# Kernel optimization log

Measured on AMD Instinct MI355X. Metric: run time of the kernel, lower is better.

The kernel has to match this reference:

```python
import jax, jax.numpy as jnp
import numpy as np

RANK, A1, A2, B1, B2 = 64, 64, 64, 64, 64
N_TOKENS = 8192


def _xavier_uniform(key, shape, fan_in, fan_out, dtype=jnp.float32):
    bound = float(np.sqrt(6.0 / (fan_in + fan_out)))
    return jax.random.uniform(key, shape, dtype, -bound, bound)


def setup_inputs() -> dict:
    key = jax.random.key(0)
    kx, ka, kb, kbias = jax.random.split(key, 4)
    x = jax.random.normal(kx, (N_TOKENS, A1 * B1), dtype=jnp.float32)
    # torch xavier on a 3D tensor (rank, d1, d2): fan_in = d1*d2, fan_out = rank*d2
    a = _xavier_uniform(ka, (RANK, A1, A2), A1 * A2, RANK * A2)
    b = _xavier_uniform(kb, (RANK, B1, B2), B1 * B2, RANK * B2)
    bias = jax.random.normal(kbias, (A2 * B2,), dtype=jnp.float32)
    return {"x": x, "a": a, "b": b, "bias": bias}


def reference(x, a, b, bias):
    r, a1, a2 = a.shape
    _, b1, b2 = b.shape
    # w = sum_r kron(a_r, b_r):  w[i*b1+k, j*b2+l] = sum_r a[r,i,j] * b[r,k,l]
    w = jnp.einsum('rij,rkl->ikjl', a, b).reshape(a1 * b1, a2 * b2)
    out = x @ w  # (N, a2*b2)
    return out + bias[None, :]
```

## Files before the change

kernel.cpp:

```cpp
#include <hip/hip_runtime.h>
#include <hip/hip_bf16.h>


#define M_DIM 8192
#define N_DIM 4096
#define K_DIM 4096
#define KT_COUNT 128

typedef __attribute__((ext_vector_type(8))) short short8;
typedef __attribute__((ext_vector_type(4))) float floatx4;

typedef __attribute__((address_space(1))) void gvoid_t;
typedef __attribute__((address_space(3))) void lvoid_t;

static __device__ __forceinline__ void gl_lds16(const void* g, const void* l) {
  __builtin_amdgcn_global_load_lds((gvoid_t*)(unsigned long long)g,
                                   (lvoid_t*)(unsigned int)(unsigned long long)l,
                                   16, 0, 0);
}

static __device__ __forceinline__ unsigned short f2bf(float f) {
  unsigned int u = __builtin_bit_cast(unsigned int, f);
  u = (u + 0x7fffu + ((u >> 16) & 1u)) >> 16;
  return (unsigned short)u;
}

#define BAR() asm volatile("s_barrier" ::: "memory")
#define WAIT_VM(N) asm volatile("s_waitcnt vmcnt(" #N ")" ::: "memory")
#define WAIT_LGKM0() asm volatile("s_waitcnt lgkmcnt(0)" ::: "memory")

__global__ __launch_bounds__(256) void build_w_kernel(
    const float* __restrict__ a, const float* __restrict__ b,
    unsigned short* __restrict__ Wp) {
  __shared__ float lds_a[1024];
  __shared__ float lds_b[2][4096];
  const int bid = blockIdx.x;
  const int t = threadIdx.x;
  const int rg = bid & 255;
  const int i = rg >> 2;
  const int j0 = (rg & 3) * 16;
  const int k0 = (bid >> 8) * 8;

  {
    const int r = t >> 2, jq = t & 3;
    float4 v = ((const float4*)(a + (size_t)r * 4096 + i * 64 + j0))[jq];
    ((float4*)lds_a)[r * 4 + jq] = v;
  }

  const float* bsrc = b + k0 * 64;

#pragma unroll
  for (int p = 0; p < 4; ++p) {
    const int idx = p * 256 + t;
    gl_lds16(bsrc + (size_t)(idx >> 7) * 4096 + (idx & 127) * 4,
             &((float4*)lds_b[0])[idx]);
  }
  WAIT_VM(0);
  __syncthreads();

  const int l = t & 63;
  const int jj = t >> 6;
  float acc[4][8];
#pragma unroll
  for (int jp = 0; jp < 4; ++jp)
#pragma unroll
    for (int kb = 0; kb < 8; ++kb) acc[jp][kb] = 0.f;

  for (int g = 0; g < 8; ++g) {
    const int cur = g & 1;
    if (g < 7) {
      const float* nb = bsrc + (size_t)(g + 1) * 8 * 4096;
#pragma unroll
      for (int p = 0; p < 4; ++p) {
        const int idx = p * 256 + t;
        gl_lds16(nb + (size_t)(idx >> 7) * 4096 + (idx & 127) * 4,
                 &((float4*)lds_b[cur ^ 1])[idx]);
      }
    }
#pragma unroll
    for (int rr = 0; rr < 8; ++rr) {
      float4 aj = ((const float4*)lds_a)[(g * 8 + rr) * 4 + jj];
      float bv[8];
#pragma unroll
      for (int kb = 0; kb < 8; ++kb) bv[kb] = lds_b[cur][rr * 512 + kb * 64 + l];
      const float av[4] = {aj.x, aj.y, aj.z, aj.w};
#pragma unroll
      for (int jp = 0; jp < 4; ++jp)
#pragma unroll
        for (int kb = 0; kb < 8; ++kb)
          acc[jp][kb] = fmaf(av[jp], bv[kb], acc[jp][kb]);
    }
    WAIT_VM(0);
    __syncthreads();
  }

  const int kt = (i * 64 + k0) >> 5;
  const int cw = (k0 & 31) >> 3;
#pragma unroll
  for (int jp = 0; jp < 4; ++jp) {
    const int j = j0 + jj * 4 + jp;
    const int n = j * 64 + l;
    const int blob = (n >> 7) * KT_COUNT + kt;
    const int pos = cw * 128 + (n & 127);
    short8 o;
#pragma unroll
    for (int kb = 0; kb < 8; ++kb) o[kb] = (short)f2bf(acc[jp][kb]);
    *(short8*)(Wp + (size_t)blob * 4096 + pos * 8) = o;
  }
}

__global__ __launch_bounds__(512) void pack_x_kernel(
    const float* __restrict__ x, unsigned short* __restrict__ Xp) {
  __shared__ short8 smem[2048];
  const int pid = blockIdx.x;
  const int M0 = pid >> 5;
  const int h = (pid >> 4) & 1;
  const int kg = pid & 15;
  const int t = threadIdx.x;

  {
    const int rsub = t >> 5;
    const int col8 = t & 31;
#pragma unroll
    for (int p = 0; p < 4; ++p) {
      const int rr = p * 16 + rsub;
      const float* src =
          x + (size_t)(M0 * 128 + h * 64 + rr) * K_DIM + kg * 256 + col8 * 8;
      float4 v0 = ((const float4*)src)[0];
      float4 v1 = ((const float4*)src)[1];
      short8 o;
      o[0] = (short)f2bf(v0.x); o[1] = (short)f2bf(v0.y);
      o[2] = (short)f2bf(v0.z); o[3] = (short)f2bf(v0.w);
      o[4] = (short)f2bf(v1.x); o[5] = (short)f2bf(v1.y);
      o[6] = (short)f2bf(v1.z); o[7] = (short)f2bf(v1.w);
      smem[rr * 32 + (col8 ^ (rr & 31))] = o;
    }
  }
  __syncthreads();

  const int ml = t & 63;
  const int c = (t >> 6) & 3;
  const int qh = t >> 8;
#pragma unroll
  for (int q = 0; q < 4; ++q) {
    const int qq = q * 2 + qh;
    const int cc = qq * 4 + c;
    short8 v = smem[ml * 32 + (cc ^ (ml & 31))];
    unsigned short* dst = Xp + (size_t)(M0 * KT_COUNT + kg * 8 + qq) * 4096 +
                          (size_t)(c * 128 + h * 64 + ml) * 8;
    *(short8*)dst = v;
  }
}

__global__ __launch_bounds__(512, 2) void gemm_kernel(
    const unsigned short* __restrict__ Xp, const unsigned short* __restrict__ Wp,
    const float* __restrict__ bias, float* __restrict__ out) {
  __shared__ short8 As[4][2][512];
  __shared__ short8 Bs[4][2][512];

  const int bid = blockIdx.x;
  const int xcd = bid & 7;
  const int pos = bid >> 3;
  const int N0 = xcd * 2 + (pos & 1);
  const int M0 = pos >> 1;

  const int t = threadIdx.x;
  const int wave = t >> 6, lane = t & 63;
  const int l16 = lane & 15, quad = lane >> 4;
  const int wm = wave & 1;
  const int wn = wave >> 1;

  floatx4 acc[8][4];
#pragma unroll
  for (int mt = 0; mt < 8; ++mt)
#pragma unroll
    for (int nt = 0; nt < 4; ++nt) acc[mt][nt] = (floatx4){0.f, 0.f, 0.f, 0.f};

  const unsigned short* gA0 = Xp + (size_t)(M0 * 2 + 0) * KT_COUNT * 4096 + (size_t)t * 8;
  const unsigned short* gA1 = Xp + (size_t)(M0 * 2 + 1) * KT_COUNT * 4096 + (size_t)t * 8;
  const unsigned short* gB0 = Wp + (size_t)(N0 * 2 + 0) * KT_COUNT * 4096 + (size_t)t * 8;
  const unsigned short* gB1 = Wp + (size_t)(N0 * 2 + 1) * KT_COUNT * 4096 + (size_t)t * 8;

  gl_lds16(gA0, &As[0][0][t]);
  gl_lds16(gA1, &As[0][1][t]);
  gl_lds16(gB0, &Bs[0][0][t]);
  gl_lds16(gB1, &Bs[0][1][t]);
  gl_lds16(gA0 + 4096, &As[1][0][t]);
  gl_lds16(gA1 + 4096, &As[1][1][t]);
  gl_lds16(gB0 + 4096, &Bs[1][0][t]);
  gl_lds16(gB1 + 4096, &Bs[1][1][t]);
  WAIT_VM(4);
  BAR();

  const int ra = quad * 128 + l16;
  const int rb = quad * 128 + (wn & 1) * 64 + l16;
  const int bh = wn >> 1;

#pragma unroll 2
  for (int kt = 0; kt < KT_COUNT; ++kt) {
    const int tb = kt & 3;
    const int db = (kt + 2) & 3;
    const size_t soff =
        (size_t)((kt + 2 < KT_COUNT) ? kt + 2 : KT_COUNT - 1) * 4096;

    short8 bf[4], af[4];

#pragma unroll
    for (int nt = 0; nt < 4; ++nt) bf[nt] = Bs[tb][bh][rb + nt * 16];
#pragma unroll
    for (int m = 0; m < 4; ++m) af[m] = As[tb][wm][ra + m * 16];
    gl_lds16(gA0 + soff, &As[db][0][t]);
    gl_lds16(gA1 + soff, &As[db][1][t]);
    BAR();
    WAIT_LGKM0();
    __builtin_amdgcn_sched_barrier(0);
    __builtin_amdgcn_s_setprio(1);
#pragma unroll
    for (int m = 0; m < 4; ++m)
#pragma unroll
      for (int nt = 0; nt < 4; ++nt)
        acc[m][nt] = __builtin_amdgcn_mfma_f32_16x16x32_bf16(
            af[m], bf[nt], acc[m][nt], 0, 0, 0);
    __builtin_amdgcn_s_setprio(0);
    __builtin_amdgcn_sched_barrier(0);
    BAR();

#pragma unroll
    for (int m = 0; m < 4; ++m) af[m] = As[tb][wm][ra + (4 + m) * 16];
    gl_lds16(gB0 + soff, &Bs[db][0][t]);
    gl_lds16(gB1 + soff, &Bs[db][1][t]);
    WAIT_VM(4);
    BAR();
    WAIT_LGKM0();
    __builtin_amdgcn_sched_barrier(0);
    __builtin_amdgcn_s_setprio(1);
#pragma unroll
    for (int m = 0; m < 4; ++m)
#pragma unroll
      for (int nt = 0; nt < 4; ++nt)
        acc[4 + m][nt] = __builtin_amdgcn_mfma_f32_16x16x32_bf16(
            af[m], bf[nt], acc[4 + m][nt], 0, 0, 0);
    __builtin_amdgcn_s_setprio(0);
    __builtin_amdgcn_sched_barrier(0);
    BAR();
  }

  const int col_base = N0 * 256 + wn * 64;
  const int row_base = M0 * 256 + wm * 128;
#pragma unroll
  for (int nt = 0; nt < 4; ++nt) {
    const int col = col_base + nt * 16 + l16;
    const float bv = bias[col];
#pragma unroll
    for (int mt = 0; mt < 8; ++mt) {
      floatx4 v = acc[mt][nt];
#pragma unroll
      for (int r4 = 0; r4 < 4; ++r4) {
        const int row = row_base + mt * 16 + quad * 4 + r4;
        out[(size_t)row * N_DIM + col] = v[r4] + bv;
      }
    }
  }
}

extern "C" void kernel_launch(void* const* d_in, const int* in_sizes, int n_in,
                              void* d_out, int out_size, void* d_ws, size_t ws_size,
                              hipStream_t stream) {
  const float* x = (const float*)d_in[0];
  const float* a = (const float*)d_in[1];
  const float* b = (const float*)d_in[2];
  const float* bias = (const float*)d_in[3];
  float* out = (float*)d_out;

  unsigned short* Xp = (unsigned short*)d_ws;
  unsigned short* Wp = Xp + (size_t)M_DIM * K_DIM;

  build_w_kernel<<<2048, 256, 0, stream>>>(a, b, Wp);
  pack_x_kernel<<<2048, 512, 0, stream>>>(x, Xp);
  gemm_kernel<<<512, 512, 0, stream>>>(Xp, Wp, bias, out);
}
```

Measured before the change: 474.2 us.

## Restructure W build for register reuse and enlarge X pack tiles

Result: slower. 489.9 us (+3.3%).

```diff
diff --git a/kernel.cpp b/kernel.cpp
--- a/kernel.cpp
+++ b/kernel.cpp
@@ -29,92 +29,92 @@
 #define WAIT_VM(N) asm volatile("s_waitcnt vmcnt(" #N ")" ::: "memory")
 #define WAIT_LGKM0() asm volatile("s_waitcnt lgkmcnt(0)" ::: "memory")
 
-__global__ __launch_bounds__(256) void build_w_kernel(
+__global__ __launch_bounds__(512, 2) void build_w_kernel(
     const float* __restrict__ a, const float* __restrict__ b,
     unsigned short* __restrict__ Wp) {
-  __shared__ float lds_a[1024];
-  __shared__ float lds_b[2][4096];
+  __shared__ float lds_a[4096];
   const int bid = blockIdx.x;
+  const int i = bid >> 2;
+  const int kq = bid & 3;
   const int t = threadIdx.x;
-  const int rg = bid & 255;
-  const int i = rg >> 2;
-  const int j0 = (rg & 3) * 16;
-  const int k0 = (bid >> 8) * 8;
-
-  {
-    const int r = t >> 2, jq = t & 3;
-    float4 v = ((const float4*)(a + (size_t)r * 4096 + i * 64 + j0))[jq];
-    ((float4*)lds_a)[r * 4 + jq] = v;
-  }
-
-  const float* bsrc = b + k0 * 64;
-
-#pragma unroll
-  for (int p = 0; p < 4; ++p) {
-    const int idx = p * 256 + t;
-    gl_lds16(bsrc + (size_t)(idx >> 7) * 4096 + (idx & 127) * 4,
-             &((float4*)lds_b[0])[idx]);
+  const int kbh = t >> 8;
+  const int j4 = (t >> 4) & 15;
+  const int l4 = t & 15;
+
+#pragma unroll
+  for (int p = 0; p < 2; ++p) {
+    const int idx = p * 512 + t;
+    const int r = idx >> 4, jq = idx & 15;
+    gl_lds16(a + (size_t)r * 4096 + i * 64 + jq * 4, &((float4*)lds_a)[idx]);
   }
   WAIT_VM(0);
   __syncthreads();
 
-  const int l = t & 63;
-  const int jj = t >> 6;
-  float acc[4][8];
+  float acc[4][4][8];
 #pragma unroll
   for (int jp = 0; jp < 4; ++jp)
 #pragma unroll
-    for (int kb = 0; kb < 8; ++kb) acc[jp][kb] = 0.f;
-
-  for (int g = 0; g < 8; ++g) {
-    const int cur = g & 1;
-    if (g < 7) {
-      const float* nb = bsrc + (size_t)(g + 1) * 8 * 4096;
-#pragma unroll
-      for (int p = 0; p < 4; ++p) {
-        const int idx = p * 256 + t;
-        gl_lds16(nb + (size_t)(idx >> 7) * 4096 + (idx & 127) * 4,
-                 &((float4*)lds_b[cur ^ 1])[idx]);
-      }
+    for (int lp = 0; lp < 4; ++lp)
+#pragma unroll
+      for (int kbi = 0; kbi < 8; ++kbi) acc[jp][lp][kbi] = 0.f;
+
+  const float* bb = b + (kq * 16 + kbh * 8) * 64 + l4 * 4;
+
+  float4 bv0[8], bv1[8];
+#pragma unroll
+  for (int kbi = 0; kbi < 8; ++kbi)
+    bv0[kbi] = *(const float4*)(bb + kbi * 64);
+
+#define BW_FMA(AV, BV)                                                   \
+  do {                                                                   \
+    const float av_[4] = {(AV).x, (AV).y, (AV).z, (AV).w};               \
+    _Pragma("unroll") for (int jp = 0; jp < 4; ++jp) {                   \
+      _Pragma("unroll") for (int kbi = 0; kbi < 8; ++kbi) {              \
+        acc[jp][0][kbi] = fmaf(av_[jp], (BV)[kbi].x, acc[jp][0][kbi]);   \
+        acc[jp][1][kbi] = fmaf(av_[jp], (BV)[kbi].y, acc[jp][1][kbi]);   \
+        acc[jp][2][kbi] = fmaf(av_[jp], (BV)[kbi].z, acc[jp][2][kbi]);   \
+        acc[jp][3][kbi] = fmaf(av_[jp], (BV)[kbi].w, acc[jp][3][kbi]);   \
+      }                                                                  \
+    }                                                                    \
+  } while (0)
+
+  for (int r = 0; r < 64; r += 2) {
+    const float* b1 = bb + (size_t)(r + 1) * 4096;
+#pragma unroll
+    for (int kbi = 0; kbi < 8; ++kbi) bv1[kbi] = *(const float4*)(b1 + kbi * 64);
+    float4 av0 = *(const float4*)&lds_a[r * 64 + j4 * 4];
+    BW_FMA(av0, bv0);
+    const int r2 = (r + 2 < 64) ? r + 2 : 0;
+    const float* b2 = bb + (size_t)r2 * 4096;
+#pragma unroll
+    for (int kbi = 0; kbi < 8; ++kbi) bv0[kbi] = *(const float4*)(b2 + kbi * 64);
+    float4 av1 = *(const float4*)&lds_a[(r + 1) * 64 + j4 * 4];
+    BW_FMA(av1, bv1);
+  }
+#undef BW_FMA
+
+  const int kt = i * 2 + (kq >> 1);
+  const int c = (kq & 1) * 2 + kbh;
+#pragma unroll
+  for (int jp = 0; jp < 4; ++jp) {
+#pragma unroll
+    for (int lp = 0; lp < 4; ++lp) {
+      const int n = (j4 * 4 + jp) * 64 + l4 * 4 + lp;
+      const int blob = (n >> 7) * KT_COUNT + kt;
+      const int pos = c * 128 + (n & 127);
+      short8 o;
+#pragma unroll
+      for (int kbi = 0; kbi < 8; ++kbi) o[kbi] = (short)f2bf(acc[jp][lp][kbi]);
+      *(short8*)(Wp + (size_t)blob * 4096 + pos * 8) = o;
     }
-#pragma unroll
-    for (int rr = 0; rr < 8; ++rr) {
-      float4 aj = ((const float4*)lds_a)[(g * 8 + rr) * 4 + jj];
-      float bv[8];
-#pragma unroll
-      for (int kb = 0; kb < 8; ++kb) bv[kb] = lds_b[cur][rr * 512 + kb * 64 + l];
-      const float av[4] = {aj.x, aj.y, aj.z, aj.w};
-#pragma unroll
-      for (int jp = 0; jp < 4; ++jp)
-#pragma unroll
-        for (int kb = 0; kb < 8; ++kb)
-          acc[jp][kb] = fmaf(av[jp], bv[kb], acc[jp][kb]);
-    }
-    WAIT_VM(0);
-    __syncthreads();
-  }
-
-  const int kt = (i * 64 + k0) >> 5;
-  const int cw = (k0 & 31) >> 3;
-#pragma unroll
-  for (int jp = 0; jp < 4; ++jp) {
-    const int j = j0 + jj * 4 + jp;
-    const int n = j * 64 + l;
-    const int blob = (n >> 7) * KT_COUNT + kt;
-    const int pos = cw * 128 + (n & 127);
-    short8 o;
-#pragma unroll
-    for (int kb = 0; kb < 8; ++kb) o[kb] = (short)f2bf(acc[jp][kb]);
-    *(short8*)(Wp + (size_t)blob * 4096 + pos * 8) = o;
   }
 }
 
 __global__ __launch_bounds__(512) void pack_x_kernel(
     const float* __restrict__ x, unsigned short* __restrict__ Xp) {
-  __shared__ short8 smem[2048];
+  __shared__ short8 smem[4096];
   const int pid = blockIdx.x;
-  const int M0 = pid >> 5;
-  const int h = (pid >> 4) & 1;
+  const int M0 = pid >> 4;
   const int kg = pid & 15;
   const int t = threadIdx.x;
 
@@ -122,10 +122,10 @@
     const int rsub = t >> 5;
     const int col8 = t & 31;
 #pragma unroll
-    for (int p = 0; p < 4; ++p) {
+    for (int p = 0; p < 8; ++p) {
       const int rr = p * 16 + rsub;
       const float* src =
-          x + (size_t)(M0 * 128 + h * 64 + rr) * K_DIM + kg * 256 + col8 * 8;
+          x + (size_t)(M0 * 128 + rr) * K_DIM + kg * 256 + col8 * 8;
       float4 v0 = ((const float4*)src)[0];
       float4 v1 = ((const float4*)src)[1];
       short8 o;
@@ -138,17 +138,12 @@
   }
   __syncthreads();
 
-  const int ml = t & 63;
-  const int c = (t >> 6) & 3;
-  const int qh = t >> 8;
-#pragma unroll
-  for (int q = 0; q < 4; ++q) {
-    const int qq = q * 2 + qh;
-    const int cc = qq * 4 + c;
-    short8 v = smem[ml * 32 + (cc ^ (ml & 31))];
-    unsigned short* dst = Xp + (size_t)(M0 * KT_COUNT + kg * 8 + qq) * 4096 +
-                          (size_t)(c * 128 + h * 64 + ml) * 8;
-    *(short8*)dst = v;
+  const int c = t >> 7, mm = t & 127;
+  unsigned short* dst = Xp + (size_t)(M0 * KT_COUNT + kg * 8) * 4096 + t * 8;
+#pragma unroll
+  for (int qq = 0; qq < 8; ++qq) {
+    short8 v = smem[mm * 32 + ((qq * 4 + c) ^ (mm & 31))];
+    *(short8*)(dst + (size_t)qq * 4096) = v;
   }
 }
 
@@ -275,7 +270,7 @@
   unsigned short* Xp = (unsigned short*)d_ws;
   unsigned short* Wp = Xp + (size_t)M_DIM * K_DIM;
 
-  build_w_kernel<<<2048, 256, 0, stream>>>(a, b, Wp);
-  pack_x_kernel<<<2048, 512, 0, stream>>>(x, Xp);
+  build_w_kernel<<<256, 512, 0, stream>>>(a, b, Wp);
+  pack_x_kernel<<<1024, 512, 0, stream>>>(x, Xp);
   gemm_kernel<<<512, 512, 0, stream>>>(Xp, Wp, bias, out);
 }
```
